# Performance work log

Measured on AMD Instinct MI355X. Metric: run time of the kernel, lower is better.

The kernel has to match this reference:

```python
import jax, jax.numpy as jnp
import numpy as np

EPS_IN = 1e-5   # InstanceNorm1d eps
EPS_DM = 1e-8   # demodulation eps


def _dcoef(weight, style):
    # rsqrt(sum_i (W[o,i]*s[b,i])^2 + eps) -> [B, out]
    return jax.lax.rsqrt(jnp.einsum('oi,bi->bo', jnp.square(weight), jnp.square(style)) + EPS_DM)


def setup_inputs() -> dict:
    key = jax.random.key(0)
    ks = jax.random.split(key, 7)
    B, S, H = 8, 1024, 1024
    lim = 1.0 / np.sqrt(H)
    u = lambda k, shp: jax.random.uniform(k, shp, jnp.float32, -lim, lim)
    return {
        'x': jax.random.normal(ks[0], (B, S, H), jnp.float32),
        'q_weight': u(ks[1], (H, H)),
        'k_weight': u(ks[2], (H, H)),
        'v_weight': u(ks[3], (H, H)),
        'w_weight': u(ks[4], (H, H)),
        'u_weight': u(ks[5], (H, H)),
        'styles': jax.random.normal(ks[6], (B, 2 * H), jnp.float32) * 0.5 + 1.0,
        'num_heads': 16,
    }


def reference(x, q_weight, k_weight, v_weight, w_weight, u_weight, styles, num_heads):
    B, S, H = x.shape
    nh = num_heads
    d = H // nh
    scale = jnp.asarray(d, x.dtype) ** -0.5

    s1 = styles[:, :H]   # modulates input hidden dim of q/k/v
    s2 = styles[:, H:]   # modulates input hidden dim of w/u and v output

    # per-sample modulation + InstanceNorm over hidden dim
    x = x * s1[:, None, :]
    mu = jnp.mean(x, axis=-1, keepdims=True)
    var = jnp.mean(jnp.square(x - mu), axis=-1, keepdims=True)
    x = (x - mu) * jax.lax.rsqrt(var + EPS_IN)

    q_dc = _dcoef(q_weight, s1)  # [B,H]
    k_dc = _dcoef(k_weight, s1)
    v_dc = _dcoef(v_weight, s1)
    w_dc = _dcoef(w_weight, s2)
    u_dc = _dcoef(u_weight, s2)

    def heads(t):  # [B,S,H] -> [B,nh,S,d]
        return t.reshape(B, S, nh, d).transpose(0, 2, 1, 3)

    q = heads(jnp.einsum('bsh,oh->bso', x, q_weight) * q_dc[:, None, :])
    k = heads(jnp.einsum('bsh,oh->bso', x, k_weight) * k_dc[:, None, :])
    v_flat = jnp.einsum('bsh,oh->bso', x, v_weight) * v_dc[:, None, :] * s2[:, None, :]
    skip = v_flat
    v = heads(v_flat)

    attn = jnp.einsum('bhqd,bhkd->bhqk', q, k) * scale
    attn = jax.nn.softmax(attn, axis=-1)
    out = jnp.einsum('bhqk,bhkd->bhqd', attn, v).transpose(0, 2, 1, 3).reshape(B, S, H)

    out = jnp.einsum('bsh,oh->bso', out, w_weight) * w_dc[:, None, :]
    skip = jnp.einsum('bsh,oh->bso', skip, u_weight) * u_dc[:, None, :]
    return out + skip
```

## Files before the change

kernel.cpp:

```cpp
#include <hip/hip_runtime.h>
#include <hip/hip_bf16.h>

#define B_ 8
#define S_ 1024
#define H_ 1024
#define NH 16
#define DH 64
#define BS (B_*S_)
#define L2E 1.44269504f

typedef unsigned short u16;
typedef __attribute__((ext_vector_type(8))) short bf16x8;
typedef __attribute__((ext_vector_type(4))) float f32x4;
typedef __attribute__((ext_vector_type(16))) float f32x16;
typedef __attribute__((ext_vector_type(4))) u16 u16x4;
typedef __attribute__((ext_vector_type(2))) unsigned int u32x2;

#define MFMA(a,b,c)   __builtin_amdgcn_mfma_f32_16x16x32_bf16((a),(b),(c),0,0,0)
#define MFMA32(a,b,c) __builtin_amdgcn_mfma_f32_32x32x16_bf16((a),(b),(c),0,0,0)

__device__ __forceinline__ u16 f2bf(float f) {
  union { float f; unsigned u; } v; v.f = f;
  unsigned r = v.u + 0x7fffu + ((v.u >> 16) & 1u);
  return (u16)(r >> 16);
}

__device__ __forceinline__ unsigned packbf2(float a, float b) {
  union { __hip_bfloat162 h; unsigned u; } v;
  v.h = __float22bfloat162_rn(float2{a, b});
  return v.u;
}

__device__ __forceinline__ void gload16(const u16* g, u16* l) {
  __builtin_amdgcn_global_load_lds(
      (const __attribute__((address_space(1))) unsigned int*)g,
      (__attribute__((address_space(3))) unsigned int*)l, 16, 0, 0);
}

__global__ __launch_bounds__(256) void dcoef_kernel(
    const float* __restrict__ qw, const float* __restrict__ kw,
    const float* __restrict__ vw, const float* __restrict__ ww,
    const float* __restrict__ uw, const float* __restrict__ styles,
    float* __restrict__ dc, u16* __restrict__ w16) {
  int bi = blockIdx.x;
  int wsel = bi >> 10;
  int o = bi & 1023;
  const float* W = (wsel == 0) ? qw : (wsel == 1) ? kw : (wsel == 2) ? vw
                   : (wsel == 3) ? ww : uw;
  int soff = (wsel < 3) ? 0 : H_;
  int tid = threadIdx.x;
  float4 w4 = *(const float4*)(W + (size_t)o * H_ + tid * 4);
  u16x4 wo = { f2bf(w4.x), f2bf(w4.y), f2bf(w4.z), f2bf(w4.w) };
  *(u16x4*)(w16 + (size_t)wsel * H_ * H_ + (size_t)o * H_ + tid * 4) = wo;
  float w2x = w4.x * w4.x, w2y = w4.y * w4.y, w2z = w4.z * w4.z, w2w = w4.w * w4.w;
  float acc[8];
#pragma unroll
  for (int b = 0; b < 8; b++) {
    float4 s4 = *(const float4*)(styles + (size_t)b * 2 * H_ + soff + tid * 4);
    acc[b] = w2x * s4.x * s4.x + w2y * s4.y * s4.y + w2z * s4.z * s4.z + w2w * s4.w * s4.w;
  }
#pragma unroll
  for (int off = 1; off < 64; off <<= 1)
#pragma unroll
    for (int b = 0; b < 8; b++) acc[b] += __shfl_xor(acc[b], off);
  __shared__ float red[4][8];
  int w = tid >> 6, l = tid & 63;
  if (l == 0)
#pragma unroll
    for (int b = 0; b < 8; b++) red[w][b] = acc[b];
  __syncthreads();
  if (tid < 8) {
    int b = tid;
    float v = red[0][b] + red[1][b] + red[2][b] + red[3][b];
    float r = rsqrtf(v + 1e-8f);
    if (wsel == 2) r *= styles[(size_t)b * 2 * H_ + H_ + o];
    dc[(size_t)wsel * B_ * H_ + b * H_ + o] = r;
  }
}

__global__ __launch_bounds__(256) void ln_kernel(
    const float* __restrict__ x, const float* __restrict__ styles,
    u16* __restrict__ xn) {
  int row = blockIdx.x;
  int b = row >> 10;
  int tid = threadIdx.x;
  const float4 xv = *(const float4*)(x + (size_t)row * H_ + tid * 4);
  const float4 sv = *(const float4*)(styles + (size_t)b * 2 * H_ + tid * 4);
  float v0 = xv.x * sv.x, v1 = xv.y * sv.y, v2 = xv.z * sv.z, v3 = xv.w * sv.w;
  float sum = v0 + v1 + v2 + v3;
  float sq = v0 * v0 + v1 * v1 + v2 * v2 + v3 * v3;
#pragma unroll
  for (int off = 1; off < 64; off <<= 1) {
    sum += __shfl_xor(sum, off);
    sq += __shfl_xor(sq, off);
  }
  __shared__ float rsum[4], rsq[4];
  int w = tid >> 6;
  if ((tid & 63) == 0) { rsum[w] = sum; rsq[w] = sq; }
  __syncthreads();
  sum = rsum[0] + rsum[1] + rsum[2] + rsum[3];
  sq = rsq[0] + rsq[1] + rsq[2] + rsq[3];
  float mean = sum * (1.f / H_);
  float var = sq * (1.f / H_) - mean * mean;
  float rstd = rsqrtf(var + 1e-5f);
  u16x4 o = { f2bf((v0 - mean) * rstd), f2bf((v1 - mean) * rstd),
              f2bf((v2 - mean) * rstd), f2bf((v3 - mean) * rstd) };
  *(u16x4*)(xn + (size_t)row * H_ + tid * 4) = o;
}

__device__ __forceinline__ void gemm128_core(
    const u16* __restrict__ Arow, const u16* __restrict__ Brow, int K,
    u16* ldsA, u16* ldsB, f32x4 acc[4][4]) {
  const int tid = threadIdx.x;
  const int l = tid & 63, w = tid >> 6;
  const int wm = (w >> 1) * 64, wn = (w & 1) * 64;
  const int lrow = l & 15, lko = (l >> 4) * 8;
  const int srow = tid >> 2;
  const int scol = (tid & 3) * 8;
  for (int k0 = 0; k0 < K; k0 += 32) {
    __syncthreads();
    gload16(Arow + (size_t)srow * K + k0 + scol,        ldsA + srow * 32 + scol);
    gload16(Arow + (size_t)(srow + 64) * K + k0 + scol, ldsA + (srow + 64) * 32 + scol);
    gload16(Brow + (size_t)srow * K + k0 + scol,        ldsB + srow * 32 + scol);
    gload16(Brow + (size_t)(srow + 64) * K + k0 + scol, ldsB + (srow + 64) * 32 + scol);
    __syncthreads();
    bf16x8 af[4], bfr[4];
#pragma unroll
    for (int i = 0; i < 4; i++)
      af[i] = *(const bf16x8*)&ldsA[(wm + i * 16 + lrow) * 32 + lko];
#pragma unroll
    for (int i = 0; i < 4; i++)
      bfr[i] = *(const bf16x8*)&ldsB[(wn + i * 16 + lrow) * 32 + lko];
#pragma unroll
    for (int mi = 0; mi < 4; mi++)
#pragma unroll
      for (int ni = 0; ni < 4; ni++)
        acc[mi][ni] = MFMA(af[mi], bfr[ni], acc[mi][ni]);
  }
}

__global__ __launch_bounds__(256) void qkv_kernel(
    const u16* __restrict__ xn, const u16* __restrict__ w16,
    const float* __restrict__ dc, u16* __restrict__ Qb, u16* __restrict__ Kb,
    u16* __restrict__ VT, u16* __restrict__ vfl) {
  __shared__ u16 ldsA[128 * 32], ldsB[128 * 32];
  int bm = blockIdx.x;
  int bn = blockIdx.y;
  f32x4 acc[4][4] = {};
  gemm128_core(xn + (size_t)bm * 128 * H_, w16 + (size_t)bn * 128 * H_, H_,
               ldsA, ldsB, acc);
  int l = threadIdx.x & 63, w = threadIdx.x >> 6;
  int wm = (w >> 1) * 64, wn = (w & 1) * 64;
  int wsel = bn >> 3;
  int col0 = (bn & 7) * 128 + wn;
  int row0 = bm * 128 + wm;
  const float* dcw = dc + (size_t)wsel * B_ * H_;
  float extra = (wsel == 0) ? 0.125f * L2E : 1.0f;
#pragma unroll
  for (int mi = 0; mi < 4; mi++) {
#pragma unroll
    for (int ni = 0; ni < 4; ni++) {
      int col = col0 + ni * 16 + (l & 15);
      int hh = col >> 6, dd = col & 63;
      int s_base = (row0 + mi * 16 + (l >> 4) * 4) & 1023;
      int b = (row0 + mi * 16 + (l >> 4) * 4) >> 10;
      float dcv = dcw[b * H_ + col] * extra;
      u16 bv[4];
#pragma unroll
      for (int rr = 0; rr < 4; rr++)
        bv[rr] = f2bf(acc[mi][ni][rr] * dcv);
      if (wsel == 0) {
#pragma unroll
        for (int rr = 0; rr < 4; rr++)
          Qb[((size_t)(b * NH + hh) * S_ + s_base + rr) * DH + dd] = bv[rr];
      } else if (wsel == 1) {
#pragma unroll
        for (int rr = 0; rr < 4; rr++)
          Kb[((size_t)(b * NH + hh) * S_ + s_base + rr) * DH + dd] = bv[rr];
      } else {
        u16x4 pv = { bv[0], bv[1], bv[2], bv[3] };
        *(u16x4*)&VT[((size_t)(b * NH + hh) * DH + dd) * S_ + s_base] = pv;
#pragma unroll
        for (int rr = 0; rr < 4; rr++)
          vfl[(size_t)(row0 + mi * 16 + (l >> 4) * 4 + rr) * H_ + col] = bv[rr];
      }
    }
  }
}

__global__ __launch_bounds__(512) void attn_kernel(
    const u16* __restrict__ Qb, const u16* __restrict__ Kb,
    const u16* __restrict__ VT, u16* __restrict__ xat) {
  __shared__ u16 ldsK[3][64 * 64];
  __shared__ u16 ldsV[3][64 * 64];
  int tid = threadIdx.x;
  int l = tid & 63, w = tid >> 6;
  int id = blockIdx.x;
  int r = id & 7, rest = id >> 3;
  int qblk = rest & 3, a = rest >> 2;
  int hl = a * 8 + r;
  int h = hl & 15, b = hl >> 4;
  int q0 = qblk * 256 + w * 32;
  const u16* Qp = Qb + ((size_t)(b * NH + h) * S_ + q0) * DH;
  const u16* Kp = Kb + (size_t)(b * NH + h) * S_ * DH;
  const u16* Vp = VT + (size_t)(b * NH + h) * DH * S_;
  int lq = l & 31, hi = l >> 5;
  int srow = tid >> 3, schunk = tid & 7;
  int ssw = (schunk * 8) ^ ((srow & 7) << 3);
  const u16* Ksrc = Kp + (size_t)srow * DH + ssw;
  const u16* Vsrc = Vp + (size_t)srow * S_ + ssw;
  int sdst = srow * 64 + schunk * 8;
  gload16(Ksrc, &ldsK[0][sdst]);
  gload16(Vsrc, &ldsV[0][sdst]);
  gload16(Ksrc + 64 * DH, &ldsK[1][sdst]);
  gload16(Vsrc + 64,      &ldsV[1][sdst]);
  bf16x8 qf[4];
#pragma unroll
  for (int s = 0; s < 4; s++)
    qf[s] = *(const bf16x8*)(Qp + lq * 64 + s * 16 + hi * 8);
  f32x16 acc0 = {}, acc1 = {};
  float ls = 0.f;
  asm volatile("s_waitcnt vmcnt(2)" ::: "memory");
  __builtin_amdgcn_s_barrier();
  int cur = 0;
  for (int t = 0; t < 16; ++t) {
    if (t + 2 < 16) {
      int nb = cur + 2; if (nb >= 3) nb -= 3;
      gload16(Ksrc + (size_t)(t + 2) * 64 * DH, &ldsK[nb][sdst]);
      gload16(Vsrc + (size_t)(t + 2) * 64,      &ldsV[nb][sdst]);
    }
    const u16* Kt = &ldsK[cur][0];
    const u16* Vt = &ldsV[cur][0];
    f32x16 z0 = {}, z1 = {};
    __builtin_amdgcn_s_setprio(1);
#pragma unroll
    for (int s = 0; s < 4; s++) {
      int ch = ((s * 2 + hi) ^ (lq & 7)) * 8;
      bf16x8 kf0 = *(const bf16x8*)&Kt[lq * 64 + ch];
      bf16x8 kf1 = *(const bf16x8*)&Kt[(32 + lq) * 64 + ch];
      z0 = MFMA32(kf0, qf[s], z0);
      z1 = MFMA32(kf1, qf[s], z1);
    }
    __builtin_amdgcn_s_setprio(0);
    float rs = 0.f;
#pragma unroll
    for (int i = 0; i < 16; i++) {
      z0[i] = __builtin_exp2f(z0[i]); rs += z0[i];
      z1[i] = __builtin_exp2f(z1[i]); rs += z1[i];
    }
    rs += __shfl_xor(rs, 32);
    ls += rs;
    bf16x8 pf[4];
#pragma unroll
    for (int g = 0; g < 2; g++) {
      unsigned pa = packbf2(z0[g * 8 + 0], z0[g * 8 + 1]);
      unsigned pb = packbf2(z0[g * 8 + 2], z0[g * 8 + 3]);
      unsigned pc = packbf2(z0[g * 8 + 4], z0[g * 8 + 5]);
      unsigned pd = packbf2(z0[g * 8 + 6], z0[g * 8 + 7]);
      u32x2 sA = __builtin_amdgcn_permlane32_swap(pa, pc, false, false);
      u32x2 sB = __builtin_amdgcn_permlane32_swap(pb, pd, false, false);
      union { unsigned u[4]; bf16x8 v; } uu;
      uu.u[0] = sA[0]; uu.u[1] = sB[0]; uu.u[2] = sA[1]; uu.u[3] = sB[1];
      pf[g] = uu.v;
    }
#pragma unroll
    for (int g = 0; g < 2; g++) {
      unsigned pa = packbf2(z1[g * 8 + 0], z1[g * 8 + 1]);
      unsigned pb = packbf2(z1[g * 8 + 2], z1[g * 8 + 3]);
      unsigned pc = packbf2(z1[g * 8 + 4], z1[g * 8 + 5]);
      unsigned pd = packbf2(z1[g * 8 + 6], z1[g * 8 + 7]);
      u32x2 sA = __builtin_amdgcn_permlane32_swap(pa, pc, false, false);
      u32x2 sB = __builtin_amdgcn_permlane32_swap(pb, pd, false, false);
      union { unsigned u[4]; bf16x8 v; } uu;
      uu.u[0] = sA[0]; uu.u[1] = sB[0]; uu.u[2] = sA[1]; uu.u[3] = sB[1];
      pf[2 + g] = uu.v;
    }
    __builtin_amdgcn_s_setprio(1);
#pragma unroll
    for (int ks = 0; ks < 4; ks++) {
      int ch = ((ks * 2 + hi) ^ (lq & 7)) * 8;
      bf16x8 vf0 = *(const bf16x8*)&Vt[lq * 64 + ch];
      bf16x8 vf1 = *(const bf16x8*)&Vt[(32 + lq) * 64 + ch];
      acc0 = MFMA32(vf0, pf[ks], acc0);
      acc1 = MFMA32(vf1, pf[ks], acc1);
    }
    __builtin_amdgcn_s_setprio(0);
    if (t < 14) {
      asm volatile("s_waitcnt vmcnt(2)" ::: "memory");
    } else if (t == 14) {
      asm volatile("s_waitcnt vmcnt(0)" ::: "memory");
    }
    if (t < 15) __builtin_amdgcn_s_barrier();
    cur = (cur == 2) ? 0 : cur + 1;
  }
  float inv = 1.f / ls;
  size_t orow = ((size_t)b * S_ + q0 + lq) * H_ + h * DH;
#pragma unroll
  for (int g = 0; g < 4; g++) {
    int d0 = g * 8 + hi * 4;
    u16x4 o0 = { f2bf(acc0[g * 4 + 0] * inv), f2bf(acc0[g * 4 + 1] * inv),
                 f2bf(acc0[g * 4 + 2] * inv), f2bf(acc0[g * 4 + 3] * inv) };
    *(u16x4*)(xat + orow + d0) = o0;
    u16x4 o1 = { f2bf(acc1[g * 4 + 0] * inv), f2bf(acc1[g * 4 + 1] * inv),
                 f2bf(acc1[g * 4 + 2] * inv), f2bf(acc1[g * 4 + 3] * inv) };
    *(u16x4*)(xat + orow + 32 + d0) = o1;
  }
}

__global__ __launch_bounds__(256) void out_kernel(
    const u16* __restrict__ xat, const u16* __restrict__ vfl,
    const u16* __restrict__ w16, const float* __restrict__ dc,
    float* __restrict__ out) {
  __shared__ u16 ldsA[128 * 32], ldsB[128 * 32];
  int bm = blockIdx.x;
  int bn = blockIdx.y;
  f32x4 acc[4][4] = {};
  gemm128_core(xat + (size_t)bm * 128 * H_,
               w16 + (size_t)3 * H_ * H_ + (size_t)bn * 128 * H_, H_,
               ldsA, ldsB, acc);
  int l = threadIdx.x & 63, w = threadIdx.x >> 6;
  int wm = (w >> 1) * 64, wn = (w & 1) * 64;
  int col0 = bn * 128 + wn;
  int row0 = bm * 128 + wm;
  int b = row0 >> 10;
  const float* wdc = dc + (size_t)3 * B_ * H_ + b * H_;
  const float* udc = dc + (size_t)4 * B_ * H_ + b * H_;
  float ratio[4], ud[4];
#pragma unroll
  for (int ni = 0; ni < 4; ni++) {
    int col = col0 + ni * 16 + (l & 15);
    ud[ni] = udc[col];
    ratio[ni] = wdc[col] / ud[ni];
  }
#pragma unroll
  for (int mi = 0; mi < 4; mi++)
#pragma unroll
    for (int ni = 0; ni < 4; ni++)
#pragma unroll
      for (int rr = 0; rr < 4; rr++) acc[mi][ni][rr] *= ratio[ni];
  gemm128_core(vfl + (size_t)bm * 128 * H_,
               w16 + (size_t)4 * H_ * H_ + (size_t)bn * 128 * H_, H_,
               ldsA, ldsB, acc);
#pragma unroll
  for (int mi = 0; mi < 4; mi++)
#pragma unroll
    for (int ni = 0; ni < 4; ni++) {
      int col = col0 + ni * 16 + (l & 15);
#pragma unroll
      for (int rr = 0; rr < 4; rr++) {
        int row = row0 + mi * 16 + (l >> 4) * 4 + rr;
        out[(size_t)row * H_ + col] = acc[mi][ni][rr] * ud[ni];
      }
    }
}

extern "C" void kernel_launch(void* const* d_in, const int* in_sizes, int n_in,
                              void* d_out, int out_size, void* d_ws, size_t ws_size,
                              hipStream_t stream) {
  const float* x = (const float*)d_in[0];
  const float* qw = (const float*)d_in[1];
  const float* kw = (const float*)d_in[2];
  const float* vw = (const float*)d_in[3];
  const float* ww = (const float*)d_in[4];
  const float* uw = (const float*)d_in[5];
  const float* styles = (const float*)d_in[6];
  float* out = (float*)d_out;

  char* ws = (char*)d_ws;
  size_t need = 163840 + (size_t)5 * H_ * H_ * 2 + (size_t)6 * BS * H_ * 2;
  if (ws_size < need) return;
  float* dc = (float*)ws;
  u16* w16 = (u16*)(ws + 163840);
  u16* xn  = w16 + (size_t)5 * H_ * H_;
  u16* Qb  = xn + (size_t)BS * H_;
  u16* Kb  = Qb + (size_t)BS * H_;
  u16* VT  = Kb + (size_t)BS * H_;
  u16* vfl = VT + (size_t)BS * H_;
  u16* xat = vfl + (size_t)BS * H_;

  dcoef_kernel<<<dim3(5 * H_), dim3(256), 0, stream>>>(qw, kw, vw, ww, uw, styles, dc, w16);
  ln_kernel<<<dim3(BS), dim3(256), 0, stream>>>(x, styles, xn);
  qkv_kernel<<<dim3(64, 24), dim3(256), 0, stream>>>(xn, w16, dc, Qb, Kb, VT, vfl);
  attn_kernel<<<dim3(512), dim3(512), 0, stream>>>(Qb, Kb, VT, xat);
  out_kernel<<<dim3(64, 8), dim3(256), 0, stream>>>(xat, vfl, w16, dc, out);
}
```

Before: 201.8 us.

## Use 2-wave 128x128 GEMM tiles with XOR-swizzled LDS layout

The 128x128 GEMM tiles in the QKV and output projections now use 2 waves of 128 threads instead of 4, each computing a 128x64 sub-tile with 8x4 MFMA accumulators. The A fragment is reused across 4 B fragments per load. The LDS staging layout changes to 64-element rows with an XOR swizzle, meant to avoid bank conflicts on the fragment reads. In exchange, per-wave register pressure roughly doubles and there are fewer threads to issue the global-to-LDS copies, which may reduce occupancy and latency hiding.

Result: slower. 212.5 us (+5.3%).

```diff
diff --git a/kernel.cpp b/kernel.cpp
--- a/kernel.cpp
+++ b/kernel.cpp
@@ -108,62 +108,74 @@
   *(u16x4*)(xn + (size_t)row * H_ + tid * 4) = o;
 }
 
-__device__ __forceinline__ void gemm128_core(
-    const u16* __restrict__ Arow, const u16* __restrict__ Brow, int K,
-    u16* ldsA, u16* ldsB, f32x4 acc[4][4]) {
+__device__ __forceinline__ void stage128(const u16* __restrict__ src, int K,
+                                         u16* dst, int tid) {
+  int ch = tid & 7;
+  int rbase = tid >> 3;
+#pragma unroll
+  for (int i = 0; i < 4; i++) {
+    int lrow = i * 16 + rbase;
+    int lch = ch ^ (lrow & 7);
+    int grow = lrow * 2 + (lch >> 2);
+    gload16(src + (size_t)grow * K + (lch & 3) * 8, dst + lrow * 64 + ch * 8);
+  }
+}
+
+__device__ __forceinline__ void gemm128_w2(
+    const u16* __restrict__ A, const u16* __restrict__ B, int K,
+    u16* ldsA, u16* ldsB, f32x4 acc[8][4]) {
   const int tid = threadIdx.x;
   const int l = tid & 63, w = tid >> 6;
-  const int wm = (w >> 1) * 64, wn = (w & 1) * 64;
-  const int lrow = l & 15, lko = (l >> 4) * 8;
-  const int srow = tid >> 2;
-  const int scol = (tid & 3) * 8;
+  const int wn = w * 64;
+  const int lrow = l & 15, kc = l >> 4;
   for (int k0 = 0; k0 < K; k0 += 32) {
     __syncthreads();
-    gload16(Arow + (size_t)srow * K + k0 + scol,        ldsA + srow * 32 + scol);
-    gload16(Arow + (size_t)(srow + 64) * K + k0 + scol, ldsA + (srow + 64) * 32 + scol);
-    gload16(Brow + (size_t)srow * K + k0 + scol,        ldsB + srow * 32 + scol);
-    gload16(Brow + (size_t)(srow + 64) * K + k0 + scol, ldsB + (srow + 64) * 32 + scol);
+    stage128(A + k0, K, ldsA, tid);
+    stage128(B + k0, K, ldsB, tid);
     __syncthreads();
-    bf16x8 af[4], bfr[4];
-#pragma unroll
-    for (int i = 0; i < 4; i++)
-      af[i] = *(const bf16x8*)&ldsA[(wm + i * 16 + lrow) * 32 + lko];
-#pragma unroll
-    for (int i = 0; i < 4; i++)
-      bfr[i] = *(const bf16x8*)&ldsB[(wn + i * 16 + lrow) * 32 + lko];
-#pragma unroll
-    for (int mi = 0; mi < 4; mi++)
+    bf16x8 bfr[4];
+#pragma unroll
+    for (int i = 0; i < 4; i++) {
+      int y = wn + i * 16 + lrow;
+      int ch = (((y & 1) << 2) | kc) ^ ((y >> 1) & 7);
+      bfr[i] = *(const bf16x8*)&ldsB[(y >> 1) * 64 + ch * 8];
+    }
+#pragma unroll
+    for (int mi = 0; mi < 8; mi++) {
+      int x = mi * 16 + lrow;
+      int ch = (((x & 1) << 2) | kc) ^ ((x >> 1) & 7);
+      bf16x8 af = *(const bf16x8*)&ldsA[(x >> 1) * 64 + ch * 8];
 #pragma unroll
       for (int ni = 0; ni < 4; ni++)
-        acc[mi][ni] = MFMA(af[mi], bfr[ni], acc[mi][ni]);
-  }
-}
-
-__global__ __launch_bounds__(256) void qkv_kernel(
+        acc[mi][ni] = MFMA(af, bfr[ni], acc[mi][ni]);
+    }
+  }
+}
+
+__global__ __launch_bounds__(128, 2) void qkv_kernel(
     const u16* __restrict__ xn, const u16* __restrict__ w16,
     const float* __restrict__ dc, u16* __restrict__ Qb, u16* __restrict__ Kb,
     u16* __restrict__ VT, u16* __restrict__ vfl) {
-  __shared__ u16 ldsA[128 * 32], ldsB[128 * 32];
+  __shared__ u16 ldsA[64 * 64], ldsB[64 * 64];
   int bm = blockIdx.x;
   int bn = blockIdx.y;
-  f32x4 acc[4][4] = {};
-  gemm128_core(xn + (size_t)bm * 128 * H_, w16 + (size_t)bn * 128 * H_, H_,
-               ldsA, ldsB, acc);
+  f32x4 acc[8][4] = {};
+  gemm128_w2(xn + (size_t)bm * 128 * H_, w16 + (size_t)bn * 128 * H_, H_,
+             ldsA, ldsB, acc);
   int l = threadIdx.x & 63, w = threadIdx.x >> 6;
-  int wm = (w >> 1) * 64, wn = (w & 1) * 64;
   int wsel = bn >> 3;
-  int col0 = (bn & 7) * 128 + wn;
-  int row0 = bm * 128 + wm;
+  int col0 = (bn & 7) * 128 + w * 64;
+  int row0 = bm * 128;
   const float* dcw = dc + (size_t)wsel * B_ * H_;
   float extra = (wsel == 0) ? 0.125f * L2E : 1.0f;
 #pragma unroll
-  for (int mi = 0; mi < 4; mi++) {
+  for (int mi = 0; mi < 8; mi++) {
+    int row = row0 + mi * 16 + (l >> 4) * 4;
+    int b = row >> 10, s_base = row & 1023;
 #pragma unroll
     for (int ni = 0; ni < 4; ni++) {
       int col = col0 + ni * 16 + (l & 15);
       int hh = col >> 6, dd = col & 63;
-      int s_base = (row0 + mi * 16 + (l >> 4) * 4) & 1023;
-      int b = (row0 + mi * 16 + (l >> 4) * 4) >> 10;
       float dcv = dcw[b * H_ + col] * extra;
       u16 bv[4];
 #pragma unroll
@@ -182,7 +194,7 @@
         *(u16x4*)&VT[((size_t)(b * NH + hh) * DH + dd) * S_ + s_base] = pv;
 #pragma unroll
         for (int rr = 0; rr < 4; rr++)
-          vfl[(size_t)(row0 + mi * 16 + (l >> 4) * 4 + rr) * H_ + col] = bv[rr];
+          vfl[(size_t)(row + rr) * H_ + col] = bv[rr];
       }
     }
   }
@@ -307,21 +319,20 @@
   }
 }
 
-__global__ __launch_bounds__(256) void out_kernel(
+__global__ __launch_bounds__(128, 2) void out_kernel(
     const u16* __restrict__ xat, const u16* __restrict__ vfl,
     const u16* __restrict__ w16, const float* __restrict__ dc,
     float* __restrict__ out) {
-  __shared__ u16 ldsA[128 * 32], ldsB[128 * 32];
+  __shared__ u16 ldsA[64 * 64], ldsB[64 * 64];
   int bm = blockIdx.x;
   int bn = blockIdx.y;
-  f32x4 acc[4][4] = {};
-  gemm128_core(xat + (size_t)bm * 128 * H_,
-               w16 + (size_t)3 * H_ * H_ + (size_t)bn * 128 * H_, H_,
-               ldsA, ldsB, acc);
+  f32x4 acc[8][4] = {};
+  gemm128_w2(xat + (size_t)bm * 128 * H_,
+             w16 + (size_t)3 * H_ * H_ + (size_t)bn * 128 * H_, H_,
+             ldsA, ldsB, acc);
   int l = threadIdx.x & 63, w = threadIdx.x >> 6;
-  int wm = (w >> 1) * 64, wn = (w & 1) * 64;
-  int col0 = bn * 128 + wn;
-  int row0 = bm * 128 + wm;
+  int col0 = bn * 128 + w * 64;
+  int row0 = bm * 128;
   int b = row0 >> 10;
   const float* wdc = dc + (size_t)3 * B_ * H_ + b * H_;
   const float* udc = dc + (size_t)4 * B_ * H_ + b * H_;
@@ -333,25 +344,25 @@
     ratio[ni] = wdc[col] / ud[ni];
   }
 #pragma unroll
-  for (int mi = 0; mi < 4; mi++)
+  for (int mi = 0; mi < 8; mi++)
 #pragma unroll
     for (int ni = 0; ni < 4; ni++)
 #pragma unroll
       for (int rr = 0; rr < 4; rr++) acc[mi][ni][rr] *= ratio[ni];
-  gemm128_core(vfl + (size_t)bm * 128 * H_,
-               w16 + (size_t)4 * H_ * H_ + (size_t)bn * 128 * H_, H_,
-               ldsA, ldsB, acc);
-#pragma unroll
-  for (int mi = 0; mi < 4; mi++)
+  gemm128_w2(vfl + (size_t)bm * 128 * H_,
+             w16 + (size_t)4 * H_ * H_ + (size_t)bn * 128 * H_, H_,
+             ldsA, ldsB, acc);
+#pragma unroll
+  for (int mi = 0; mi < 8; mi++) {
+    int row = row0 + mi * 16 + (l >> 4) * 4;
 #pragma unroll
     for (int ni = 0; ni < 4; ni++) {
       int col = col0 + ni * 16 + (l & 15);
 #pragma unroll
-      for (int rr = 0; rr < 4; rr++) {
-        int row = row0 + mi * 16 + (l >> 4) * 4 + rr;
-        out[(size_t)row * H_ + col] = acc[mi][ni][rr] * ud[ni];
-      }
-    }
+      for (int rr = 0; rr < 4; rr++)
+        out[(size_t)(row + rr) * H_ + col] = acc[mi][ni][rr] * ud[ni];
+    }
+  }
 }
 
 extern "C" void kernel_launch(void* const* d_in, const int* in_sizes, int n_in,
@@ -380,7 +391,7 @@
 
   dcoef_kernel<<<dim3(5 * H_), dim3(256), 0, stream>>>(qw, kw, vw, ww, uw, styles, dc, w16);
   ln_kernel<<<dim3(BS), dim3(256), 0, stream>>>(x, styles, xn);
-  qkv_kernel<<<dim3(64, 24), dim3(256), 0, stream>>>(xn, w16, dc, Qb, Kb, VT, vfl);
+  qkv_kernel<<<dim3(64, 24), dim3(128), 0, stream>>>(xn, w16, dc, Qb, Kb, VT, vfl);
   attn_kernel<<<dim3(512), dim3(512), 0, stream>>>(Qb, Kb, VT, xat);
-  out_kernel<<<dim3(64, 8), dim3(256), 0, stream>>>(xat, vfl, w16, dc, out);
-}
+  out_kernel<<<dim3(64, 8), dim3(128), 0, stream>>>(xat, vfl, w16, dc, out);
+}
```

## Rewrite QKV GEMM with 256x128 tiles, triple-buffered async LDS staging and swizzle

Applied to the files above, without the earlier changes.

Replaces the QKV projection GEMM with a 256x128 tile per block, where each wave computes 128x64. It triple-buffers global-to-LDS loads with explicit vmcnt waits so loads overlap the MFMAs, and uses an XOR-swizzled LDS layout to avoid bank conflicts. It also raises MFMA priority during compute. The larger tile improves data reuse and halves the grid, at the cost of more registers (32 accumulators) and LDS, plus a smaller grid that may underfill the GPU.

Result: slower. 211.0 us (+4.6%).

```diff
diff --git a/kernel.cpp b/kernel.cpp
--- a/kernel.cpp
+++ b/kernel.cpp
@@ -108,6 +108,115 @@
   *(u16x4*)(xn + (size_t)row * H_ + tid * 4) = o;
 }
 
+__device__ __forceinline__ void stageBlk(const u16* __restrict__ src,
+                                         u16* dst, int tid) {
+#pragma unroll
+  for (int i = 0; i < 2; i++) {
+    int lr2 = i * 32 + (tid >> 3);
+    int ch = tid & 7;
+    int lch = ch ^ (lr2 & 7);
+    int grow = lr2 * 2 + (lch >> 2);
+    gload16(src + (size_t)grow * H_ + (lch & 3) * 8, dst + lr2 * 64 + ch * 8);
+  }
+}
+
+__global__ __launch_bounds__(256, 2) void qkv_kernel(
+    const u16* __restrict__ xn, const u16* __restrict__ w16,
+    const float* __restrict__ dc, u16* __restrict__ Qb, u16* __restrict__ Kb,
+    u16* __restrict__ VT, u16* __restrict__ vfl) {
+  __shared__ u16 ldsA[3][2][64 * 64];
+  __shared__ u16 ldsB[3][64 * 64];
+  int bm = blockIdx.x;
+  int bn = blockIdx.y;
+  const u16* A  = xn + (size_t)bm * 256 * H_;
+  const u16* Bp = w16 + (size_t)bn * 128 * H_;
+  int tid = threadIdx.x;
+  int l = tid & 63, w = tid >> 6;
+  int wr = w >> 1, wc = w & 1;
+  int lrow = l & 15, kc = l >> 4;
+  f32x4 acc[8][4] = {};
+  stageBlk(A,                    ldsA[0][0], tid);
+  stageBlk(A + (size_t)128 * H_, ldsA[0][1], tid);
+  stageBlk(Bp,                   ldsB[0],    tid);
+  stageBlk(A + 32,                    ldsA[1][0], tid);
+  stageBlk(A + (size_t)128 * H_ + 32, ldsA[1][1], tid);
+  stageBlk(Bp + 32,                   ldsB[1],    tid);
+  asm volatile("s_waitcnt vmcnt(6)" ::: "memory");
+  __builtin_amdgcn_s_barrier();
+  int bufc = 0;
+  for (int t = 0; t < 32; ++t) {
+    if (t + 2 < 32) {
+      int nb = bufc + 2; if (nb >= 3) nb -= 3;
+      const u16* As = A + (t + 2) * 32;
+      stageBlk(As,                    ldsA[nb][0], tid);
+      stageBlk(As + (size_t)128 * H_, ldsA[nb][1], tid);
+      stageBlk(Bp + (t + 2) * 32,     ldsB[nb],    tid);
+    }
+    const u16* At = ldsA[bufc][wr];
+    const u16* Bt = ldsB[bufc];
+    bf16x8 bfr[4];
+#pragma unroll
+    for (int i = 0; i < 4; i++) {
+      int y = wc * 64 + i * 16 + lrow;
+      int ch = (((y & 1) << 2) | kc) ^ ((y >> 1) & 7);
+      bfr[i] = *(const bf16x8*)&Bt[(y >> 1) * 64 + ch * 8];
+    }
+    __builtin_amdgcn_s_setprio(1);
+#pragma unroll
+    for (int mi = 0; mi < 8; mi++) {
+      int x = mi * 16 + lrow;
+      int ch = (((x & 1) << 2) | kc) ^ ((x >> 1) & 7);
+      bf16x8 af = *(const bf16x8*)&At[(x >> 1) * 64 + ch * 8];
+#pragma unroll
+      for (int ni = 0; ni < 4; ni++)
+        acc[mi][ni] = MFMA(af, bfr[ni], acc[mi][ni]);
+    }
+    __builtin_amdgcn_s_setprio(0);
+    if (t + 2 < 32) {
+      asm volatile("s_waitcnt vmcnt(6)" ::: "memory");
+    } else if (t == 30) {
+      asm volatile("s_waitcnt vmcnt(0)" ::: "memory");
+    }
+    __builtin_amdgcn_s_barrier();
+    bufc = (bufc == 2) ? 0 : bufc + 1;
+  }
+  int wsel = bn >> 3;
+  int col0 = (bn & 7) * 128 + wc * 64;
+  int row0 = bm * 256 + wr * 128;
+  const float* dcw = dc + (size_t)wsel * B_ * H_;
+  float extra = (wsel == 0) ? 0.125f * L2E : 1.0f;
+#pragma unroll
+  for (int mi = 0; mi < 8; mi++) {
+    int row = row0 + mi * 16 + (l >> 4) * 4;
+    int b = row >> 10, s_base = row & 1023;
+#pragma unroll
+    for (int ni = 0; ni < 4; ni++) {
+      int col = col0 + ni * 16 + (l & 15);
+      int hh = col >> 6, dd = col & 63;
+      float dcv = dcw[b * H_ + col] * extra;
+      u16 bv[4];
+#pragma unroll
+      for (int rr = 0; rr < 4; rr++)
+        bv[rr] = f2bf(acc[mi][ni][rr] * dcv);
+      if (wsel == 0) {
+#pragma unroll
+        for (int rr = 0; rr < 4; rr++)
+          Qb[((size_t)(b * NH + hh) * S_ + s_base + rr) * DH + dd] = bv[rr];
+      } else if (wsel == 1) {
+#pragma unroll
+        for (int rr = 0; rr < 4; rr++)
+          Kb[((size_t)(b * NH + hh) * S_ + s_base + rr) * DH + dd] = bv[rr];
+      } else {
+        u16x4 pv = { bv[0], bv[1], bv[2], bv[3] };
+        *(u16x4*)&VT[((size_t)(b * NH + hh) * DH + dd) * S_ + s_base] = pv;
+#pragma unroll
+        for (int rr = 0; rr < 4; rr++)
+          vfl[(size_t)(row + rr) * H_ + col] = bv[rr];
+      }
+    }
+  }
+}
+
 __device__ __forceinline__ void gemm128_core(
     const u16* __restrict__ Arow, const u16* __restrict__ Brow, int K,
     u16* ldsA, u16* ldsB, f32x4 acc[4][4]) {
@@ -136,55 +245,6 @@
 #pragma unroll
       for (int ni = 0; ni < 4; ni++)
         acc[mi][ni] = MFMA(af[mi], bfr[ni], acc[mi][ni]);
-  }
-}
-
-__global__ __launch_bounds__(256) void qkv_kernel(
-    const u16* __restrict__ xn, const u16* __restrict__ w16,
-    const float* __restrict__ dc, u16* __restrict__ Qb, u16* __restrict__ Kb,
-    u16* __restrict__ VT, u16* __restrict__ vfl) {
-  __shared__ u16 ldsA[128 * 32], ldsB[128 * 32];
-  int bm = blockIdx.x;
-  int bn = blockIdx.y;
-  f32x4 acc[4][4] = {};
-  gemm128_core(xn + (size_t)bm * 128 * H_, w16 + (size_t)bn * 128 * H_, H_,
-               ldsA, ldsB, acc);
-  int l = threadIdx.x & 63, w = threadIdx.x >> 6;
-  int wm = (w >> 1) * 64, wn = (w & 1) * 64;
-  int wsel = bn >> 3;
-  int col0 = (bn & 7) * 128 + wn;
-  int row0 = bm * 128 + wm;
-  const float* dcw = dc + (size_t)wsel * B_ * H_;
-  float extra = (wsel == 0) ? 0.125f * L2E : 1.0f;
-#pragma unroll
-  for (int mi = 0; mi < 4; mi++) {
-#pragma unroll
-    for (int ni = 0; ni < 4; ni++) {
-      int col = col0 + ni * 16 + (l & 15);
-      int hh = col >> 6, dd = col & 63;
-      int s_base = (row0 + mi * 16 + (l >> 4) * 4) & 1023;
-      int b = (row0 + mi * 16 + (l >> 4) * 4) >> 10;
-      float dcv = dcw[b * H_ + col] * extra;
-      u16 bv[4];
-#pragma unroll
-      for (int rr = 0; rr < 4; rr++)
-        bv[rr] = f2bf(acc[mi][ni][rr] * dcv);
-      if (wsel == 0) {
-#pragma unroll
-        for (int rr = 0; rr < 4; rr++)
-          Qb[((size_t)(b * NH + hh) * S_ + s_base + rr) * DH + dd] = bv[rr];
-      } else if (wsel == 1) {
-#pragma unroll
-        for (int rr = 0; rr < 4; rr++)
-          Kb[((size_t)(b * NH + hh) * S_ + s_base + rr) * DH + dd] = bv[rr];
-      } else {
-        u16x4 pv = { bv[0], bv[1], bv[2], bv[3] };
-        *(u16x4*)&VT[((size_t)(b * NH + hh) * DH + dd) * S_ + s_base] = pv;
-#pragma unroll
-        for (int rr = 0; rr < 4; rr++)
-          vfl[(size_t)(row0 + mi * 16 + (l >> 4) * 4 + rr) * H_ + col] = bv[rr];
-      }
-    }
   }
 }
 
@@ -380,7 +440,7 @@
 
   dcoef_kernel<<<dim3(5 * H_), dim3(256), 0, stream>>>(qw, kw, vw, ww, uw, styles, dc, w16);
   ln_kernel<<<dim3(BS), dim3(256), 0, stream>>>(x, styles, xn);
-  qkv_kernel<<<dim3(64, 24), dim3(256), 0, stream>>>(xn, w16, dc, Qb, Kb, VT, vfl);
+  qkv_kernel<<<dim3(32, 24), dim3(256), 0, stream>>>(xn, w16, dc, Qb, Kb, VT, vfl);
   attn_kernel<<<dim3(512), dim3(512), 0, stream>>>(Qb, Kb, VT, xat);
   out_kernel<<<dim3(64, 8), dim3(256), 0, stream>>>(xat, vfl, w16, dc, out);
 }
```

## Process two 32-row query tiles per wave in attention to reuse K/V fragments

Applied to the files above, without the earlier changes.

Each wave now handles 64 query rows, computed as two 32-row sets that share the K and V fragments read from LDS, so each block covers 512 queries and the grid shrinks from 512 to 256 blocks. This halves K/V global loads and LDS reads per query row and gives the MFMA units more independent work per fragment load. In exchange, register pressure roughly doubles (four score and four output accumulators), and 256 blocks may underfill a 256-CU device while also changing the block-to-head ordering used for L2 locality.

Result: slower. 205.9 us (+2.0%).

```diff
diff --git a/kernel.cpp b/kernel.cpp
--- a/kernel.cpp
+++ b/kernel.cpp
@@ -196,11 +196,10 @@
   int tid = threadIdx.x;
   int l = tid & 63, w = tid >> 6;
   int id = blockIdx.x;
-  int r = id & 7, rest = id >> 3;
-  int qblk = rest & 3, a = rest >> 2;
-  int hl = a * 8 + r;
+  int qblk = id >> 7;
+  int hl = id & 127;
   int h = hl & 15, b = hl >> 4;
-  int q0 = qblk * 256 + w * 32;
+  int q0 = qblk * 512 + w * 64;
   const u16* Qp = Qb + ((size_t)(b * NH + h) * S_ + q0) * DH;
   const u16* Kp = Kb + (size_t)(b * NH + h) * S_ * DH;
   const u16* Vp = VT + (size_t)(b * NH + h) * DH * S_;
@@ -214,12 +213,14 @@
   gload16(Vsrc, &ldsV[0][sdst]);
   gload16(Ksrc + 64 * DH, &ldsK[1][sdst]);
   gload16(Vsrc + 64,      &ldsV[1][sdst]);
-  bf16x8 qf[4];
-#pragma unroll
-  for (int s = 0; s < 4; s++)
-    qf[s] = *(const bf16x8*)(Qp + lq * 64 + s * 16 + hi * 8);
-  f32x16 acc0 = {}, acc1 = {};
-  float ls = 0.f;
+  bf16x8 qfA[4], qfB[4];
+#pragma unroll
+  for (int s = 0; s < 4; s++) {
+    qfA[s] = *(const bf16x8*)(Qp + lq * 64 + s * 16 + hi * 8);
+    qfB[s] = *(const bf16x8*)(Qp + (32 + lq) * 64 + s * 16 + hi * 8);
+  }
+  f32x16 acc0A = {}, acc1A = {}, acc0B = {}, acc1B = {};
+  float lsA = 0.f, lsB = 0.f;
   asm volatile("s_waitcnt vmcnt(2)" ::: "memory");
   __builtin_amdgcn_s_barrier();
   int cur = 0;
@@ -231,49 +232,76 @@
     }
     const u16* Kt = &ldsK[cur][0];
     const u16* Vt = &ldsV[cur][0];
-    f32x16 z0 = {}, z1 = {};
+    f32x16 z0A = {}, z1A = {}, z0B = {}, z1B = {};
     __builtin_amdgcn_s_setprio(1);
 #pragma unroll
     for (int s = 0; s < 4; s++) {
       int ch = ((s * 2 + hi) ^ (lq & 7)) * 8;
       bf16x8 kf0 = *(const bf16x8*)&Kt[lq * 64 + ch];
       bf16x8 kf1 = *(const bf16x8*)&Kt[(32 + lq) * 64 + ch];
-      z0 = MFMA32(kf0, qf[s], z0);
-      z1 = MFMA32(kf1, qf[s], z1);
+      z0A = MFMA32(kf0, qfA[s], z0A);
+      z1A = MFMA32(kf1, qfA[s], z1A);
+      z0B = MFMA32(kf0, qfB[s], z0B);
+      z1B = MFMA32(kf1, qfB[s], z1B);
     }
     __builtin_amdgcn_s_setprio(0);
-    float rs = 0.f;
+    float rsA = 0.f, rsB = 0.f;
 #pragma unroll
     for (int i = 0; i < 16; i++) {
-      z0[i] = __builtin_exp2f(z0[i]); rs += z0[i];
-      z1[i] = __builtin_exp2f(z1[i]); rs += z1[i];
-    }
-    rs += __shfl_xor(rs, 32);
-    ls += rs;
-    bf16x8 pf[4];
+      z0A[i] = __builtin_exp2f(z0A[i]); rsA += z0A[i];
+      z1A[i] = __builtin_exp2f(z1A[i]); rsA += z1A[i];
+      z0B[i] = __builtin_exp2f(z0B[i]); rsB += z0B[i];
+      z1B[i] = __builtin_exp2f(z1B[i]); rsB += z1B[i];
+    }
+    rsA += __shfl_xor(rsA, 32); lsA += rsA;
+    rsB += __shfl_xor(rsB, 32); lsB += rsB;
+    bf16x8 pfA[4], pfB[4];
 #pragma unroll
     for (int g = 0; g < 2; g++) {
-      unsigned pa = packbf2(z0[g * 8 + 0], z0[g * 8 + 1]);
-      unsigned pb = packbf2(z0[g * 8 + 2], z0[g * 8 + 3]);
-      unsigned pc = packbf2(z0[g * 8 + 4], z0[g * 8 + 5]);
-      unsigned pd = packbf2(z0[g * 8 + 6], z0[g * 8 + 7]);
-      u32x2 sA = __builtin_amdgcn_permlane32_swap(pa, pc, false, false);
-      u32x2 sB = __builtin_amdgcn_permlane32_swap(pb, pd, false, false);
-      union { unsigned u[4]; bf16x8 v; } uu;
-      uu.u[0] = sA[0]; uu.u[1] = sB[0]; uu.u[2] = sA[1]; uu.u[3] = sB[1];
-      pf[g] = uu.v;
-    }
-#pragma unroll
-    for (int g = 0; g < 2; g++) {
-      unsigned pa = packbf2(z1[g * 8 + 0], z1[g * 8 + 1]);
-      unsigned pb = packbf2(z1[g * 8 + 2], z1[g * 8 + 3]);
-      unsigned pc = packbf2(z1[g * 8 + 4], z1[g * 8 + 5]);
-      unsigned pd = packbf2(z1[g * 8 + 6], z1[g * 8 + 7]);
-      u32x2 sA = __builtin_amdgcn_permlane32_swap(pa, pc, false, false);
-      u32x2 sB = __builtin_amdgcn_permlane32_swap(pb, pd, false, false);
-      union { unsigned u[4]; bf16x8 v; } uu;
-      uu.u[0] = sA[0]; uu.u[1] = sB[0]; uu.u[2] = sA[1]; uu.u[3] = sB[1];
-      pf[2 + g] = uu.v;
+      {
+        unsigned pa = packbf2(z0A[g * 8 + 0], z0A[g * 8 + 1]);
+        unsigned pb = packbf2(z0A[g * 8 + 2], z0A[g * 8 + 3]);
+        unsigned pc = packbf2(z0A[g * 8 + 4], z0A[g * 8 + 5]);
+        unsigned pd = packbf2(z0A[g * 8 + 6], z0A[g * 8 + 7]);
+        u32x2 sA = __builtin_amdgcn_permlane32_swap(pa, pc, false, false);
+        u32x2 sB = __builtin_amdgcn_permlane32_swap(pb, pd, false, false);
+        union { unsigned u[4]; bf16x8 v; } uu;
+        uu.u[0] = sA[0]; uu.u[1] = sB[0]; uu.u[2] = sA[1]; uu.u[3] = sB[1];
+        pfA[g] = uu.v;
+      }
+      {
+        unsigned pa = packbf2(z1A[g * 8 + 0], z1A[g * 8 + 1]);
+        unsigned pb = packbf2(z1A[g * 8 + 2], z1A[g * 8 + 3]);
+        unsigned pc = packbf2(z1A[g * 8 + 4], z1A[g * 8 + 5]);
+        unsigned pd = packbf2(z1A[g * 8 + 6], z1A[g * 8 + 7]);
+        u32x2 sA = __builtin_amdgcn_permlane32_swap(pa, pc, false, false);
+        u32x2 sB = __builtin_amdgcn_permlane32_swap(pb, pd, false, false);
+        union { unsigned u[4]; bf16x8 v; } uu;
+        uu.u[0] = sA[0]; uu.u[1] = sB[0]; uu.u[2] = sA[1]; uu.u[3] = sB[1];
+        pfA[2 + g] = uu.v;
+      }
+      {
+        unsigned pa = packbf2(z0B[g * 8 + 0], z0B[g * 8 + 1]);
+        unsigned pb = packbf2(z0B[g * 8 + 2], z0B[g * 8 + 3]);
+        unsigned pc = packbf2(z0B[g * 8 + 4], z0B[g * 8 + 5]);
+        unsigned pd = packbf2(z0B[g * 8 + 6], z0B[g * 8 + 7]);
+        u32x2 sA = __builtin_amdgcn_permlane32_swap(pa, pc, false, false);
+        u32x2 sB = __builtin_amdgcn_permlane32_swap(pb, pd, false, false);
+        union { unsigned u[4]; bf16x8 v; } uu;
+        uu.u[0] = sA[0]; uu.u[1] = sB[0]; uu.u[2] = sA[1]; uu.u[3] = sB[1];
+        pfB[g] = uu.v;
+      }
+      {
+        unsigned pa = packbf2(z1B[g * 8 + 0], z1B[g * 8 + 1]);
+        unsigned pb = packbf2(z1B[g * 8 + 2], z1B[g * 8 + 3]);
+        unsigned pc = packbf2(z1B[g * 8 + 4], z1B[g * 8 + 5]);
+        unsigned pd = packbf2(z1B[g * 8 + 6], z1B[g * 8 + 7]);
+        u32x2 sA = __builtin_amdgcn_permlane32_swap(pa, pc, false, false);
+        u32x2 sB = __builtin_amdgcn_permlane32_swap(pb, pd, false, false);
+        union { unsigned u[4]; bf16x8 v; } uu;
+        uu.u[0] = sA[0]; uu.u[1] = sB[0]; uu.u[2] = sA[1]; uu.u[3] = sB[1];
+        pfB[2 + g] = uu.v;
+      }
     }
     __builtin_amdgcn_s_setprio(1);
 #pragma unroll
@@ -281,8 +309,10 @@
       int ch = ((ks * 2 + hi) ^ (lq & 7)) * 8;
       bf16x8 vf0 = *(const bf16x8*)&Vt[lq * 64 + ch];
       bf16x8 vf1 = *(const bf16x8*)&Vt[(32 + lq) * 64 + ch];
-      acc0 = MFMA32(vf0, pf[ks], acc0);
-      acc1 = MFMA32(vf1, pf[ks], acc1);
+      acc0A = MFMA32(vf0, pfA[ks], acc0A);
+      acc1A = MFMA32(vf1, pfA[ks], acc1A);
+      acc0B = MFMA32(vf0, pfB[ks], acc0B);
+      acc1B = MFMA32(vf1, pfB[ks], acc1B);
     }
     __builtin_amdgcn_s_setprio(0);
     if (t < 14) {
@@ -293,17 +323,24 @@
     if (t < 15) __builtin_amdgcn_s_barrier();
     cur = (cur == 2) ? 0 : cur + 1;
   }
-  float inv = 1.f / ls;
-  size_t orow = ((size_t)b * S_ + q0 + lq) * H_ + h * DH;
+  float invA = 1.f / lsA, invB = 1.f / lsB;
+  size_t orowA = ((size_t)b * S_ + q0 + lq) * H_ + h * DH;
+  size_t orowB = orowA + (size_t)32 * H_;
 #pragma unroll
   for (int g = 0; g < 4; g++) {
     int d0 = g * 8 + hi * 4;
-    u16x4 o0 = { f2bf(acc0[g * 4 + 0] * inv), f2bf(acc0[g * 4 + 1] * inv),
-                 f2bf(acc0[g * 4 + 2] * inv), f2bf(acc0[g * 4 + 3] * inv) };
-    *(u16x4*)(xat + orow + d0) = o0;
-    u16x4 o1 = { f2bf(acc1[g * 4 + 0] * inv), f2bf(acc1[g * 4 + 1] * inv),
-                 f2bf(acc1[g * 4 + 2] * inv), f2bf(acc1[g * 4 + 3] * inv) };
-    *(u16x4*)(xat + orow + 32 + d0) = o1;
+    u16x4 a0 = { f2bf(acc0A[g * 4 + 0] * invA), f2bf(acc0A[g * 4 + 1] * invA),
+                 f2bf(acc0A[g * 4 + 2] * invA), f2bf(acc0A[g * 4 + 3] * invA) };
+    *(u16x4*)(xat + orowA + d0) = a0;
+    u16x4 a1 = { f2bf(acc1A[g * 4 + 0] * invA), f2bf(acc1A[g * 4 + 1] * invA),
+                 f2bf(acc1A[g * 4 + 2] * invA), f2bf(acc1A[g * 4 + 3] * invA) };
+    *(u16x4*)(xat + orowA + 32 + d0) = a1;
+    u16x4 b0 = { f2bf(acc0B[g * 4 + 0] * invB), f2bf(acc0B[g * 4 + 1] * invB),
+                 f2bf(acc0B[g * 4 + 2] * invB), f2bf(acc0B[g * 4 + 3] * invB) };
+    *(u16x4*)(xat + orowB + d0) = b0;
+    u16x4 b1 = { f2bf(acc1B[g * 4 + 0] * invB), f2bf(acc1B[g * 4 + 1] * invB),
+                 f2bf(acc1B[g * 4 + 2] * invB), f2bf(acc1B[g * 4 + 3] * invB) };
+    *(u16x4*)(xat + orowB + 32 + d0) = b1;
   }
 }
 
@@ -381,6 +418,6 @@
   dcoef_kernel<<<dim3(5 * H_), dim3(256), 0, stream>>>(qw, kw, vw, ww, uw, styles, dc, w16);
   ln_kernel<<<dim3(BS), dim3(256), 0, stream>>>(x, styles, xn);
   qkv_kernel<<<dim3(64, 24), dim3(256), 0, stream>>>(xn, w16, dc, Qb, Kb, VT, vfl);
-  attn_kernel<<<dim3(512), dim3(512), 0, stream>>>(Qb, Kb, VT, xat);
+  attn_kernel<<<dim3(256), dim3(512), 0, stream>>>(Qb, Kb, VT, xat);
   out_kernel<<<dim3(64, 8), dim3(256), 0, stream>>>(xat, vfl, w16, dc, out);
 }
```
